# Kernel optimization log

Measured on AMD Instinct MI355X. Metric: run time of the kernel, lower is better.

## Reference

```python
import jax, jax.numpy as jnp
import numpy as np

D = 8
W = 256
NUM_FREQS = 10
NUM_FREQS_VIEWS = 4
SKIPS = (4,)
PE_DIM = 3 + 2 * 3 * NUM_FREQS        # 63
VE_DIM = 3 + 2 * 3 * NUM_FREQS_VIEWS  # 27
N_RAYS, N_SAMPLES = 4096, 64


def embed(x, num_freqs):
    # torch order: [x, sin(x*f0), cos(x*f0), sin(x*f1), cos(x*f1), ...]
    freqs = (2.0 ** jnp.arange(num_freqs)).astype(x.dtype)
    xf = x[..., None, :] * freqs[:, None]              # [..., F, 3]
    sc = jnp.stack([jnp.sin(xf), jnp.cos(xf)], axis=-2)  # [..., F, 2, 3]
    return jnp.concatenate([x, sc.reshape(*x.shape[:-1], num_freqs * 6)], -1)


def setup_inputs() -> dict:
    key = jax.random.key(0)
    ks = iter(jax.random.split(key, 32))
    inp = {}
    inp["input_pts"] = jax.random.normal(next(ks), (N_RAYS, N_SAMPLES, 3), jnp.float32)
    inp["input_views"] = jax.random.normal(next(ks), (N_RAYS, 3), jnp.float32)
    # pts MLP: layer 5 (index 5) takes W + PE_DIM due to skip after layer 4
    in_dims = [PE_DIM] + [(W + PE_DIM) if i in SKIPS else W for i in range(D - 1)]
    for i, d in enumerate(in_dims):
        inp[f"pts_w{i}"] = jax.random.normal(next(ks), (d, W), jnp.float32) / np.sqrt(d).astype(np.float32)
        inp[f"pts_b{i}"] = jnp.zeros((W,), jnp.float32)
    inp["views_w"] = jax.random.normal(next(ks), (VE_DIM + W, W // 2), jnp.float32) / np.sqrt(VE_DIM + W).astype(np.float32)
    inp["views_b"] = jnp.zeros((W // 2,), jnp.float32)
    inp["feat_w"] = jax.random.normal(next(ks), (W, W), jnp.float32) / np.sqrt(W).astype(np.float32)
    inp["feat_b"] = jnp.zeros((W,), jnp.float32)
    inp["alpha_w"] = jax.random.normal(next(ks), (W, 1), jnp.float32) / np.sqrt(W).astype(np.float32)
    inp["alpha_b"] = jnp.zeros((1,), jnp.float32)
    inp["rgb_w"] = jax.random.normal(next(ks), (W // 2, 3), jnp.float32) / np.sqrt(W // 2).astype(np.float32)
    inp["rgb_b"] = jnp.zeros((3,), jnp.float32)
    return inp


def reference(input_pts, input_views,
              pts_w0, pts_b0, pts_w1, pts_b1, pts_w2, pts_b2, pts_w3, pts_b3,
              pts_w4, pts_b4, pts_w5, pts_b5, pts_w6, pts_b6, pts_w7, pts_b7,
              views_w, views_b, feat_w, feat_b, alpha_w, alpha_b, rgb_w, rgb_b):
    pts_ws = [pts_w0, pts_w1, pts_w2, pts_w3, pts_w4, pts_w5, pts_w6, pts_w7]
    pts_bs = [pts_b0, pts_b1, pts_b2, pts_b3, pts_b4, pts_b5, pts_b6, pts_b7]
    R, S = input_pts.shape[0], input_pts.shape[1]
    ep = embed(input_pts, NUM_FREQS).reshape(-1, PE_DIM)            # [R*S, 63]
    ev = embed(input_views, NUM_FREQS_VIEWS)                        # [R, 27]
    ev = jnp.broadcast_to(ev[:, None, :], (R, S, VE_DIM)).reshape(-1, VE_DIM)
    h = ep
    for i in range(D):
        h = jax.nn.relu(h @ pts_ws[i] + pts_bs[i])
        if i in SKIPS:
            h = jnp.concatenate([ep, h], -1)
    alpha = h @ alpha_w + alpha_b                                    # [R*S, 1]
    feature = h @ feat_w + feat_b                                    # [R*S, W]
    h2 = jax.nn.relu(jnp.concatenate([feature, ev], -1) @ views_w + views_b)
    rgb = h2 @ rgb_w + rgb_b                                         # [R*S, 3]
    return jnp.concatenate([rgb, alpha], -1).reshape(R, S, 4)
```

## Files before the change

kernel.cpp:

```cpp
#include <hip/hip_runtime.h>

typedef _Float16 h16;
typedef __attribute__((ext_vector_type(8))) _Float16 half8;
typedef __attribute__((ext_vector_type(4))) _Float16 half4;
typedef __attribute__((ext_vector_type(4))) float f32x4;
typedef __attribute__((ext_vector_type(16))) float f32x16;

constexpr size_t OFF_P0 = 0;
constexpr size_t OFF_P1 = 16384;
constexpr size_t OFF_P2 = 81920;
constexpr size_t OFF_P3 = 147456;
constexpr size_t OFF_P4 = 212992;
constexpr size_t OFF_P5 = 278528;
constexpr size_t OFF_P6 = 360448;
constexpr size_t OFF_P7 = 425984;
constexpr size_t OFF_FEAT = 491520;
constexpr size_t OFF_VIEWS = 557056;

__device__ __forceinline__ f32x16 mfma32(half8 a, half8 b, f32x16 c) {
  return __builtin_amdgcn_mfma_f32_32x32x16_f16(a, b, c, 0, 0, 0);
}
__device__ __forceinline__ half8 ldfrag(const h16* __restrict__ base, int frag, int l) {
  return *(const half8*)(base + (size_t)frag * 512 + (size_t)l * 8);
}
__device__ __forceinline__ half8 ldsfrag(const h16* __restrict__ base, int frag, int l) {
  return *(const half8*)(base + frag * 512 + l * 8);
}

__global__ void convw_kernel(const float* __restrict__ src, h16* __restrict__ dst,
                             int Ksrc, int N, int Kp, int p, int npad) {
  int t = blockIdx.x * 256 + threadIdx.x;
  int nfrags = (Kp >> 4) * (N >> 5);
  int frag = t >> 6;
  if (frag >= nfrags) return;
  int l = t & 63;
  int ntiles = N >> 5;
  int kt = frag / ntiles;
  int nt = frag - kt * ntiles;
  int col = nt * 32 + (l & 31);
  int kbase = kt * 16 + (l >> 5) * 8;
  half8 v;
#pragma unroll
  for (int j = 0; j < 8; ++j) {
    int k = kbase + j;
    float x = 0.f;
    if (k < p) {
      x = src[(size_t)k * N + col];
    } else if (k >= p + npad) {
      int r = k - npad;
      if (r < Ksrc) x = src[(size_t)r * N + col];
    }
    v[j] = (h16)x;
  }
  *(half8*)(dst + (size_t)frag * 512 + (size_t)l * 8) = v;
}

struct Params {
  const float* pts;
  const float* views;
  const h16* wf;
  const float* pb[8];
  const float* views_b;
  const float* feat_b;
  const float* alpha_w;
  const float* alpha_b;
  const float* rgb_w;
  const float* rgb_b;
  float* out;
};

template <bool RELU>
__device__ __forceinline__ void epiW(h16* __restrict__ Y, const f32x16& A,
                                     int rt, int ct, const float* __restrict__ bias,
                                     int lr, int lh) {
#pragma unroll
  for (int g = 0; g < 4; ++g) {
    int col0 = ct * 32 + g * 8 + lh * 4;
    f32x4 bv = *(const f32x4*)(bias + col0);
    half4 pk;
#pragma unroll
    for (int i = 0; i < 4; ++i) {
      float v = A[g * 4 + i] + bv[i];
      if (RELU) v = fmaxf(v, 0.f);
      pk[i] = (h16)v;
    }
    *(half4*)(Y + (rt * 16 + ct * 2 + (g >> 1)) * 512 + ((g & 1) * 32 + lr) * 8 + lh * 4) = pk;
  }
}

__device__ __forceinline__ float embed_col(int c, float x0, float x1, float x2) {
  if (c < 3) return c == 0 ? x0 : (c == 1 ? x1 : x2);
  if (c >= 63) return 0.f;
  int t = c - 3;
  int f = t / 6, rem = t - f * 6;
  int d = rem >= 3 ? rem - 3 : rem;
  float x = (d == 0 ? x0 : (d == 1 ? x1 : x2)) * (float)(1 << f);
  return (rem < 3) ? sinf(x) : cosf(x);
}

template <int KT, bool EXTEP, bool RELU>
__device__ __forceinline__ void layerF(h16* __restrict__ h, const h16* __restrict__ ep,
                                       const h16* __restrict__ wcur,
                                       const h16* __restrict__ wnextp, int nstride,
                                       const float* __restrict__ bias,
                                       half8 (&wr)[4],
                                       int w, int l, int lr, int lh) {
  f32x16 a0 = (f32x16)0.f, a1 = (f32x16)0.f;
#pragma unroll
  for (int i = 0; i < KT; ++i) {
    half8 x0, x1;
    if (EXTEP && i < 4) {
      x0 = ldsfrag(ep, i, l);
      x1 = ldsfrag(ep, 4 + i, l);
    } else {
      const int kt = EXTEP ? i - 4 : i;
      x0 = ldsfrag(h, kt, l);
      x1 = ldsfrag(h, 16 + kt, l);
    }
    half8 b = wr[i & 3];
    if (i + 4 < KT)
      wr[i & 3] = ldfrag(wcur, (i + 4) * 8 + w, l);
    else
      wr[i & 3] = ldfrag(wnextp, (i + 4 - KT) * nstride, l);
    a0 = mfma32(b, x0, a0);
    a1 = mfma32(b, x1, a1);
  }
  __syncthreads();
  epiW<RELU>(h, a0, 0, w, bias, lr, lh);
  epiW<RELU>(h, a1, 1, w, bias, lr, lh);
  __syncthreads();
}

__global__ __launch_bounds__(512, 4) void nerf_kernel(Params P) {
  __shared__ __align__(16) h16 h[32 * 512];
  __shared__ __align__(16) h16 ep[8 * 512];
  __shared__ __align__(16) h16 evp[32];
  __shared__ float alpha_s[64];

  const int tid = threadIdx.x;
  const int w = tid >> 6, l = tid & 63;
  const int lr = l & 31, lh = l >> 5;
  const int ray = blockIdx.x;
  const h16* wf = P.wf;

  half8 wr[4];
#pragma unroll
  for (int j = 0; j < 4; ++j) wr[j] = ldfrag(wf + OFF_P0, j * 8 + w, l);

  {
    const int s = tid >> 3, q = tid & 7;
    const float* ps = P.pts + ((size_t)ray * 64 + s) * 3;
    const float x0 = ps[0], x1 = ps[1], x2 = ps[2];
    half8 v;
#pragma unroll
    for (int j = 0; j < 8; ++j)
      v[j] = (h16)embed_col(q * 8 + j, x0, x1, x2);
    *(half8*)(ep + ((s >> 5) * 4 + (q >> 1)) * 512 + ((s & 31) + 32 * (q & 1)) * 8) = v;
  }
  if (tid < 32) {
    const int idx = tid;
    float v = 0.f;
    if (idx < 27) {
      if (idx < 3) {
        v = P.views[(size_t)ray * 3 + idx];
      } else {
        const int f = (idx - 3) / 6, rem = (idx - 3) % 6, d = rem % 3;
        const float x = P.views[(size_t)ray * 3 + d] * (float)(1 << f);
        v = (rem < 3) ? sinf(x) : cosf(x);
      }
    }
    evp[idx] = (h16)v;
  }
  __syncthreads();

  {
    f32x16 a0 = (f32x16)0.f, a1 = (f32x16)0.f;
#pragma unroll
    for (int i = 0; i < 4; ++i) {
      half8 x0 = ldsfrag(ep, i, l);
      half8 x1 = ldsfrag(ep, 4 + i, l);
      half8 b = wr[i & 3];
      wr[i & 3] = ldfrag(wf + OFF_P1, i * 8 + w, l);
      a0 = mfma32(b, x0, a0);
      a1 = mfma32(b, x1, a1);
    }
    __syncthreads();
    epiW<true>(h, a0, 0, w, P.pb[0], lr, lh);
    epiW<true>(h, a1, 1, w, P.pb[0], lr, lh);
    __syncthreads();
  }

  layerF<16, false, true>(h, ep, wf + OFF_P1, wf + OFF_P2 + (size_t)w * 512, 8, P.pb[1], wr, w, l, lr, lh);
  layerF<16, false, true>(h, ep, wf + OFF_P2, wf + OFF_P3 + (size_t)w * 512, 8, P.pb[2], wr, w, l, lr, lh);
  layerF<16, false, true>(h, ep, wf + OFF_P3, wf + OFF_P4 + (size_t)w * 512, 8, P.pb[3], wr, w, l, lr, lh);
  layerF<16, false, true>(h, ep, wf + OFF_P4, wf + OFF_P5 + (size_t)w * 512, 8, P.pb[4], wr, w, l, lr, lh);
  layerF<20, true,  true>(h, ep, wf + OFF_P5, wf + OFF_P6 + (size_t)w * 512, 8, P.pb[5], wr, w, l, lr, lh);
  layerF<16, false, true>(h, ep, wf + OFF_P6, wf + OFF_P7 + (size_t)w * 512, 8, P.pb[6], wr, w, l, lr, lh);
  layerF<16, false, true>(h, ep, wf + OFF_P7, wf + OFF_FEAT + (size_t)w * 512, 8, P.pb[7], wr, w, l, lr, lh);

  {
    const int s = tid >> 3, q = tid & 7;
    float sum = 0.f;
#pragma unroll
    for (int j = 0; j < 4; ++j) {
      int k0 = q * 32 + j * 8;
      half8 hv = *(const half8*)(h + ((s >> 5) * 16 + (k0 >> 4)) * 512 +
                                 ((s & 31) + 32 * ((k0 >> 3) & 1)) * 8);
      f32x4 w0 = *(const f32x4*)(P.alpha_w + k0);
      f32x4 w1 = *(const f32x4*)(P.alpha_w + k0 + 4);
      sum += (float)hv[0] * w0[0] + (float)hv[1] * w0[1] + (float)hv[2] * w0[2] + (float)hv[3] * w0[3];
      sum += (float)hv[4] * w1[0] + (float)hv[5] * w1[1] + (float)hv[6] * w1[2] + (float)hv[7] * w1[3];
    }
    sum += __shfl_xor(sum, 1);
    sum += __shfl_xor(sum, 2);
    sum += __shfl_xor(sum, 4);
    if (q == 0) alpha_s[s] = sum + P.alpha_b[0];
  }

  layerF<16, false, false>(h, ep, wf + OFF_FEAT, wf + OFF_VIEWS + (size_t)(w & 3) * 512, 4, P.feat_b, wr, w, l, lr, lh);

  {
    const int rt = w >> 2, ct = w & 3;
    const h16* wV = wf + OFF_VIEWS;
    f32x16 acc = (f32x16)0.f;
#pragma unroll
    for (int i = 0; i < 18; ++i) {
      half8 x;
      if (i < 16) x = ldsfrag(h, rt * 16 + i, l);
      else x = *(const half8*)(evp + (i - 16) * 16 + lh * 8);
      half8 b = wr[i & 3];
      if (i + 4 < 18) wr[i & 3] = ldfrag(wV, (i + 4) * 4 + ct, l);
      acc = mfma32(b, x, acc);
    }
    __syncthreads();
    epiW<true>(h, acc, rt, ct, P.views_b, lr, lh);
    __syncthreads();
  }

  {
    const int s = tid >> 3, q = tid & 7;
    float r0 = 0.f, r1 = 0.f, r2 = 0.f;
#pragma unroll
    for (int j = 0; j < 2; ++j) {
      int k0 = q * 16 + j * 8;
      half8 hv = *(const half8*)(h + ((s >> 5) * 16 + (k0 >> 4)) * 512 +
                                 ((s & 31) + 32 * ((k0 >> 3) & 1)) * 8);
#pragma unroll
      for (int i = 0; i < 8; ++i) {
        const float f = (float)hv[i];
        r0 += f * P.rgb_w[(k0 + i) * 3 + 0];
        r1 += f * P.rgb_w[(k0 + i) * 3 + 1];
        r2 += f * P.rgb_w[(k0 + i) * 3 + 2];
      }
    }
    r0 += __shfl_xor(r0, 1); r0 += __shfl_xor(r0, 2); r0 += __shfl_xor(r0, 4);
    r1 += __shfl_xor(r1, 1); r1 += __shfl_xor(r1, 2); r1 += __shfl_xor(r1, 4);
    r2 += __shfl_xor(r2, 1); r2 += __shfl_xor(r2, 2); r2 += __shfl_xor(r2, 4);
    if (q == 0) {
      float4 o;
      o.x = r0 + P.rgb_b[0];
      o.y = r1 + P.rgb_b[1];
      o.z = r2 + P.rgb_b[2];
      o.w = alpha_s[s];
      *(float4*)(P.out + ((size_t)ray * 64 + s) * 4) = o;
    }
  }
}

extern "C" void kernel_launch(void* const* d_in, const int* in_sizes, int n_in,
                              void* d_out, int out_size, void* d_ws, size_t ws_size,
                              hipStream_t stream) {
  h16* wsw = (h16*)d_ws;
  auto conv = [&](int idx, int Ksrc, int N, int Kp, int p, int npad, size_t off) {
    int nfrags = (Kp / 16) * (N / 32);
    int total = nfrags * 64;
    convw_kernel<<<(total + 255) / 256, 256, 0, stream>>>(
        (const float*)d_in[idx], wsw + off, Ksrc, N, Kp, p, npad);
  };
  conv(2, 63, 256, 64, 63, 1, OFF_P0);
  conv(4, 256, 256, 256, 256, 0, OFF_P1);
  conv(6, 256, 256, 256, 256, 0, OFF_P2);
  conv(8, 256, 256, 256, 256, 0, OFF_P3);
  conv(10, 256, 256, 256, 256, 0, OFF_P4);
  conv(12, 319, 256, 320, 63, 1, OFF_P5);
  conv(14, 256, 256, 256, 256, 0, OFF_P6);
  conv(16, 256, 256, 256, 256, 0, OFF_P7);
  conv(20, 256, 256, 256, 256, 0, OFF_FEAT);
  conv(18, 283, 128, 288, 283, 5, OFF_VIEWS);

  Params P;
  P.pts = (const float*)d_in[0];
  P.views = (const float*)d_in[1];
  P.wf = wsw;
  for (int i = 0; i < 8; ++i) P.pb[i] = (const float*)d_in[3 + 2 * i];
  P.views_b = (const float*)d_in[19];
  P.feat_b = (const float*)d_in[21];
  P.alpha_w = (const float*)d_in[22];
  P.alpha_b = (const float*)d_in[23];
  P.rgb_w = (const float*)d_in[24];
  P.rgb_b = (const float*)d_in[25];
  P.out = (float*)d_out;

  nerf_kernel<<<4096, 512, 0, stream>>>(P);
}
```

Before: 370.0 us.

## Halve block to four waves each computing two column tiles per layer

The block shrinks from 8 to 4 waves. In each MLP layer, every wave now computes two 32-wide output column tiles with four accumulators, so each activation fragment read from LDS feeds two weight fragments. The weight prefetch depth drops from 4 to 2 per stream, and the embed, alpha and rgb reductions are rebalanced for 256 threads. This cuts LDS read traffic per MFMA and the number of synchronizing waves, but leaves fewer resident waves per CU to hide global weight-load latency.

```diff
diff --git a/kernel.cpp b/kernel.cpp
--- a/kernel.cpp
+++ b/kernel.cpp
@@ -99,13 +99,14 @@
 }
 
 template <int KT, bool EXTEP, bool RELU>
-__device__ __forceinline__ void layerF(h16* __restrict__ h, const h16* __restrict__ ep,
+__device__ __forceinline__ void layerQ(h16* __restrict__ h, const h16* __restrict__ ep,
                                        const h16* __restrict__ wcur,
-                                       const h16* __restrict__ wnextp, int nstride,
+                                       const h16* __restrict__ wnA,
+                                       const h16* __restrict__ wnB, int nstride,
                                        const float* __restrict__ bias,
-                                       half8 (&wr)[4],
-                                       int w, int l, int lr, int lh) {
-  f32x16 a0 = (f32x16)0.f, a1 = (f32x16)0.f;
+                                       half8 (&wrA)[2], half8 (&wrB)[2],
+                                       int ctA, int ctB, int l, int lr, int lh) {
+  f32x16 a0 = (f32x16)0.f, a1 = (f32x16)0.f, a2 = (f32x16)0.f, a3 = (f32x16)0.f;
 #pragma unroll
   for (int i = 0; i < KT; ++i) {
     half8 x0, x1;
@@ -117,21 +118,28 @@
       x0 = ldsfrag(h, kt, l);
       x1 = ldsfrag(h, 16 + kt, l);
     }
-    half8 b = wr[i & 3];
-    if (i + 4 < KT)
-      wr[i & 3] = ldfrag(wcur, (i + 4) * 8 + w, l);
-    else
-      wr[i & 3] = ldfrag(wnextp, (i + 4 - KT) * nstride, l);
-    a0 = mfma32(b, x0, a0);
-    a1 = mfma32(b, x1, a1);
+    half8 bA = wrA[i & 1], bB = wrB[i & 1];
+    if (i + 2 < KT) {
+      wrA[i & 1] = ldfrag(wcur, (i + 2) * 8 + ctA, l);
+      wrB[i & 1] = ldfrag(wcur, (i + 2) * 8 + ctB, l);
+    } else {
+      wrA[i & 1] = ldfrag(wnA, (i + 2 - KT) * nstride, l);
+      wrB[i & 1] = ldfrag(wnB, (i + 2 - KT) * nstride, l);
+    }
+    a0 = mfma32(bA, x0, a0);
+    a1 = mfma32(bA, x1, a1);
+    a2 = mfma32(bB, x0, a2);
+    a3 = mfma32(bB, x1, a3);
   }
   __syncthreads();
-  epiW<RELU>(h, a0, 0, w, bias, lr, lh);
-  epiW<RELU>(h, a1, 1, w, bias, lr, lh);
+  epiW<RELU>(h, a0, 0, ctA, bias, lr, lh);
+  epiW<RELU>(h, a1, 1, ctA, bias, lr, lh);
+  epiW<RELU>(h, a2, 0, ctB, bias, lr, lh);
+  epiW<RELU>(h, a3, 1, ctB, bias, lr, lh);
   __syncthreads();
 }
 
-__global__ __launch_bounds__(512, 4) void nerf_kernel(Params P) {
+__global__ __launch_bounds__(256, 3) void nerf_kernel(Params P) {
   __shared__ __align__(16) h16 h[32 * 512];
   __shared__ __align__(16) h16 ep[8 * 512];
   __shared__ __align__(16) h16 evp[32];
@@ -140,22 +148,30 @@
   const int tid = threadIdx.x;
   const int w = tid >> 6, l = tid & 63;
   const int lr = l & 31, lh = l >> 5;
+  const int ctA = 2 * w, ctB = 2 * w + 1;
   const int ray = blockIdx.x;
   const h16* wf = P.wf;
 
-  half8 wr[4];
-#pragma unroll
-  for (int j = 0; j < 4; ++j) wr[j] = ldfrag(wf + OFF_P0, j * 8 + w, l);
-
-  {
-    const int s = tid >> 3, q = tid & 7;
+  half8 wrA[2], wrB[2];
+#pragma unroll
+  for (int j = 0; j < 2; ++j) {
+    wrA[j] = ldfrag(wf + OFF_P0, j * 8 + ctA, l);
+    wrB[j] = ldfrag(wf + OFF_P0, j * 8 + ctB, l);
+  }
+
+  {
+    const int s = tid >> 2, q = tid & 3;
     const float* ps = P.pts + ((size_t)ray * 64 + s) * 3;
     const float x0 = ps[0], x1 = ps[1], x2 = ps[2];
-    half8 v;
-#pragma unroll
-    for (int j = 0; j < 8; ++j)
-      v[j] = (h16)embed_col(q * 8 + j, x0, x1, x2);
-    *(half8*)(ep + ((s >> 5) * 4 + (q >> 1)) * 512 + ((s & 31) + 32 * (q & 1)) * 8) = v;
+    half8 v0, v1;
+#pragma unroll
+    for (int j = 0; j < 8; ++j) {
+      v0[j] = (h16)embed_col(q * 16 + j, x0, x1, x2);
+      v1[j] = (h16)embed_col(q * 16 + 8 + j, x0, x1, x2);
+    }
+    h16* base = ep + ((s >> 5) * 4 + q) * 512;
+    *(half8*)(base + (s & 31) * 8) = v0;
+    *(half8*)(base + (32 + (s & 31)) * 8) = v1;
   }
   if (tid < 32) {
     const int idx = tid;
@@ -174,36 +190,45 @@
   __syncthreads();
 
   {
-    f32x16 a0 = (f32x16)0.f, a1 = (f32x16)0.f;
+    f32x16 a0 = (f32x16)0.f, a1 = (f32x16)0.f, a2 = (f32x16)0.f, a3 = (f32x16)0.f;
 #pragma unroll
     for (int i = 0; i < 4; ++i) {
       half8 x0 = ldsfrag(ep, i, l);
       half8 x1 = ldsfrag(ep, 4 + i, l);
-      half8 b = wr[i & 3];
-      wr[i & 3] = ldfrag(wf + OFF_P1, i * 8 + w, l);
-      a0 = mfma32(b, x0, a0);
-      a1 = mfma32(b, x1, a1);
-    }
+      half8 bA = wrA[i & 1], bB = wrB[i & 1];
+      if (i + 2 < 4) {
+        wrA[i & 1] = ldfrag(wf + OFF_P0, (i + 2) * 8 + ctA, l);
+        wrB[i & 1] = ldfrag(wf + OFF_P0, (i + 2) * 8 + ctB, l);
+      } else {
+        wrA[i & 1] = ldfrag(wf + OFF_P1, (i + 2 - 4) * 8 + ctA, l);
+        wrB[i & 1] = ldfrag(wf + OFF_P1, (i + 2 - 4) * 8 + ctB, l);
+      }
+      a0 = mfma32(bA, x0, a0);
+      a1 = mfma32(bA, x1, a1);
+      a2 = mfma32(bB, x0, a2);
+      a3 = mfma32(bB, x1, a3);
+    }
+    epiW<true>(h, a0, 0, ctA, P.pb[0], lr, lh);
+    epiW<true>(h, a1, 1, ctA, P.pb[0], lr, lh);
+    epiW<true>(h, a2, 0, ctB, P.pb[0], lr, lh);
+    epiW<true>(h, a3, 1, ctB, P.pb[0], lr, lh);
     __syncthreads();
-    epiW<true>(h, a0, 0, w, P.pb[0], lr, lh);
-    epiW<true>(h, a1, 1, w, P.pb[0], lr, lh);
-    __syncthreads();
-  }
-
-  layerF<16, false, true>(h, ep, wf + OFF_P1, wf + OFF_P2 + (size_t)w * 512, 8, P.pb[1], wr, w, l, lr, lh);
-  layerF<16, false, true>(h, ep, wf + OFF_P2, wf + OFF_P3 + (size_t)w * 512, 8, P.pb[2], wr, w, l, lr, lh);
-  layerF<16, false, true>(h, ep, wf + OFF_P3, wf + OFF_P4 + (size_t)w * 512, 8, P.pb[3], wr, w, l, lr, lh);
-  layerF<16, false, true>(h, ep, wf + OFF_P4, wf + OFF_P5 + (size_t)w * 512, 8, P.pb[4], wr, w, l, lr, lh);
-  layerF<20, true,  true>(h, ep, wf + OFF_P5, wf + OFF_P6 + (size_t)w * 512, 8, P.pb[5], wr, w, l, lr, lh);
-  layerF<16, false, true>(h, ep, wf + OFF_P6, wf + OFF_P7 + (size_t)w * 512, 8, P.pb[6], wr, w, l, lr, lh);
-  layerF<16, false, true>(h, ep, wf + OFF_P7, wf + OFF_FEAT + (size_t)w * 512, 8, P.pb[7], wr, w, l, lr, lh);
-
-  {
-    const int s = tid >> 3, q = tid & 7;
+  }
+
+  layerQ<16, false, true>(h, ep, wf + OFF_P1, wf + OFF_P2 + (size_t)ctA * 512, wf + OFF_P2 + (size_t)ctB * 512, 8, P.pb[1], wrA, wrB, ctA, ctB, l, lr, lh);
+  layerQ<16, false, true>(h, ep, wf + OFF_P2, wf + OFF_P3 + (size_t)ctA * 512, wf + OFF_P3 + (size_t)ctB * 512, 8, P.pb[2], wrA, wrB, ctA, ctB, l, lr, lh);
+  layerQ<16, false, true>(h, ep, wf + OFF_P3, wf + OFF_P4 + (size_t)ctA * 512, wf + OFF_P4 + (size_t)ctB * 512, 8, P.pb[3], wrA, wrB, ctA, ctB, l, lr, lh);
+  layerQ<16, false, true>(h, ep, wf + OFF_P4, wf + OFF_P5 + (size_t)ctA * 512, wf + OFF_P5 + (size_t)ctB * 512, 8, P.pb[4], wrA, wrB, ctA, ctB, l, lr, lh);
+  layerQ<20, true,  true>(h, ep, wf + OFF_P5, wf + OFF_P6 + (size_t)ctA * 512, wf + OFF_P6 + (size_t)ctB * 512, 8, P.pb[5], wrA, wrB, ctA, ctB, l, lr, lh);
+  layerQ<16, false, true>(h, ep, wf + OFF_P6, wf + OFF_P7 + (size_t)ctA * 512, wf + OFF_P7 + (size_t)ctB * 512, 8, P.pb[6], wrA, wrB, ctA, ctB, l, lr, lh);
+  layerQ<16, false, true>(h, ep, wf + OFF_P7, wf + OFF_FEAT + (size_t)ctA * 512, wf + OFF_FEAT + (size_t)ctB * 512, 8, P.pb[7], wrA, wrB, ctA, ctB, l, lr, lh);
+
+  {
+    const int s = tid >> 2, q = tid & 3;
     float sum = 0.f;
 #pragma unroll
-    for (int j = 0; j < 4; ++j) {
-      int k0 = q * 32 + j * 8;
+    for (int j = 0; j < 8; ++j) {
+      int k0 = q * 64 + j * 8;
       half8 hv = *(const half8*)(h + ((s >> 5) * 16 + (k0 >> 4)) * 512 +
                                  ((s & 31) + 32 * ((k0 >> 3) & 1)) * 8);
       f32x4 w0 = *(const f32x4*)(P.alpha_w + k0);
@@ -213,36 +238,41 @@
     }
     sum += __shfl_xor(sum, 1);
     sum += __shfl_xor(sum, 2);
-    sum += __shfl_xor(sum, 4);
     if (q == 0) alpha_s[s] = sum + P.alpha_b[0];
   }
 
-  layerF<16, false, false>(h, ep, wf + OFF_FEAT, wf + OFF_VIEWS + (size_t)(w & 3) * 512, 4, P.feat_b, wr, w, l, lr, lh);
-
-  {
-    const int rt = w >> 2, ct = w & 3;
+  layerQ<16, false, false>(h, ep, wf + OFF_FEAT, wf + OFF_VIEWS + (size_t)w * 512, wf + OFF_VIEWS + (size_t)w * 512, 4, P.feat_b, wrA, wrB, ctA, ctB, l, lr, lh);
+
+  {
     const h16* wV = wf + OFF_VIEWS;
-    f32x16 acc = (f32x16)0.f;
+    f32x16 a0 = (f32x16)0.f, a1 = (f32x16)0.f;
 #pragma unroll
     for (int i = 0; i < 18; ++i) {
-      half8 x;
-      if (i < 16) x = ldsfrag(h, rt * 16 + i, l);
-      else x = *(const half8*)(evp + (i - 16) * 16 + lh * 8);
-      half8 b = wr[i & 3];
-      if (i + 4 < 18) wr[i & 3] = ldfrag(wV, (i + 4) * 4 + ct, l);
-      acc = mfma32(b, x, acc);
+      half8 x0, x1;
+      if (i < 16) {
+        x0 = ldsfrag(h, i, l);
+        x1 = ldsfrag(h, 16 + i, l);
+      } else {
+        x0 = *(const half8*)(evp + (i - 16) * 16 + lh * 8);
+        x1 = x0;
+      }
+      half8 b = wrA[i & 1];
+      if (i + 2 < 18) wrA[i & 1] = ldfrag(wV, (i + 2) * 4 + w, l);
+      a0 = mfma32(b, x0, a0);
+      a1 = mfma32(b, x1, a1);
     }
     __syncthreads();
-    epiW<true>(h, acc, rt, ct, P.views_b, lr, lh);
+    epiW<true>(h, a0, 0, w, P.views_b, lr, lh);
+    epiW<true>(h, a1, 1, w, P.views_b, lr, lh);
     __syncthreads();
   }
 
   {
-    const int s = tid >> 3, q = tid & 7;
+    const int s = tid >> 2, q = tid & 3;
     float r0 = 0.f, r1 = 0.f, r2 = 0.f;
 #pragma unroll
-    for (int j = 0; j < 2; ++j) {
-      int k0 = q * 16 + j * 8;
+    for (int j = 0; j < 4; ++j) {
+      int k0 = q * 32 + j * 8;
       half8 hv = *(const half8*)(h + ((s >> 5) * 16 + (k0 >> 4)) * 512 +
                                  ((s & 31) + 32 * ((k0 >> 3) & 1)) * 8);
 #pragma unroll
@@ -253,9 +283,9 @@
         r2 += f * P.rgb_w[(k0 + i) * 3 + 2];
       }
     }
-    r0 += __shfl_xor(r0, 1); r0 += __shfl_xor(r0, 2); r0 += __shfl_xor(r0, 4);
-    r1 += __shfl_xor(r1, 1); r1 += __shfl_xor(r1, 2); r1 += __shfl_xor(r1, 4);
-    r2 += __shfl_xor(r2, 1); r2 += __shfl_xor(r2, 2); r2 += __shfl_xor(r2, 4);
+    r0 += __shfl_xor(r0, 1); r0 += __shfl_xor(r0, 2);
+    r1 += __shfl_xor(r1, 1); r1 += __shfl_xor(r1, 2);
+    r2 += __shfl_xor(r2, 1); r2 += __shfl_xor(r2, 2);
     if (q == 0) {
       float4 o;
       o.x = r0 + P.rgb_b[0];
@@ -301,5 +331,5 @@
   P.rgb_b = (const float*)d_in[25];
   P.out = (float*)d_out;
 
-  nerf_kernel<<<4096, 512, 0, stream>>>(P);
-}
+  nerf_kernel<<<4096, 256, 0, stream>>>(P);
+}
```

Measured after the change: 367.1 us. Within noise of the previous version (-0.8%).
